# Kernel optimization log

Hardware: AMD Instinct MI355X
Metric: run time of the kernel (lower is better)

The kernel has to match this reference:

```python
import jax, jax.numpy as jnp
import numpy as np

D_MODEL, D_STATE, EXPAND = 1024, 16, 2
D_INNER = D_MODEL * EXPAND
BATCH, SEQ = 4, 2048
DT = 0.1

def setup_inputs() -> dict:
    key = jax.random.key(0)
    ks = jax.random.split(key, 12)
    s = 0.02
    inp = {
        "x": jax.random.normal(ks[0], (BATCH, SEQ, D_MODEL), jnp.float32),
        "B_mod": jax.random.normal(ks[1], (BATCH, D_STATE), jnp.float32) * 0.1,
        "C_mod": jax.random.normal(ks[2], (BATCH, D_STATE), jnp.float32) * 0.1,
        "W_in": jax.random.normal(ks[3], (D_MODEL, 2 * D_INNER), jnp.float32) * s,
        "b_in": jnp.zeros((2 * D_INNER,), jnp.float32),
        "conv_w": jax.random.normal(ks[4], (D_INNER, 1, 3), jnp.float32) * 0.3,
        "conv_b": jnp.zeros((D_INNER,), jnp.float32),
        "A_log": jnp.tile(jnp.log(jnp.arange(1, D_STATE + 1, dtype=jnp.float32))[None, :], (D_INNER, 1)),
        "D": jnp.ones((D_INNER,), jnp.float32),
        "W_B": jax.random.normal(ks[5], (D_INNER, D_STATE), jnp.float32) * s,
        "b_B": jnp.zeros((D_STATE,), jnp.float32),
        "W_C": jax.random.normal(ks[6], (D_INNER, D_STATE), jnp.float32) * s,
        "b_C": jnp.zeros((D_STATE,), jnp.float32),
        "W_out": jax.random.normal(ks[7], (D_INNER, D_MODEL), jnp.float32) * s,
        "b_out": jnp.zeros((D_MODEL,), jnp.float32),
    }
    return inp

def _silu(v):
    return v * jax.nn.sigmoid(v)

def reference(x, B_mod, C_mod, W_in, b_in, conv_w, conv_b, A_log, D, W_B, b_B, W_C, b_C, W_out, b_out):
    # in_proj + split + gate
    xr = x @ W_in + b_in                      # (B, L, 2*D_INNER)
    x_ssm, x_res = jnp.split(xr, 2, axis=-1)
    x_ssm = _silu(x_ssm)
    # depthwise conv1d, kernel 3, padding 1
    xc = jnp.transpose(x_ssm, (0, 2, 1))      # (B, C, L)
    xc = jax.lax.conv_general_dilated(
        xc, conv_w, window_strides=(1,), padding=[(1, 1)],
        dimension_numbers=("NCH", "OIH", "NCH"), feature_group_count=D_INNER)
    xc = xc + conv_b[None, :, None]
    x_ssm = jnp.transpose(xc, (0, 2, 1))      # (B, L, D_INNER)
    # SSM params
    A = -jnp.exp(A_log)                       # (D_INNER, D_STATE)
    A_bar = jnp.exp(A * DT)
    B = x_ssm @ W_B + b_B + B_mod[:, None, :] # (B, L, D_STATE)
    C = x_ssm @ W_C + b_C + C_mod[:, None, :]
    # sequential scan over time
    def step(h, inp):
        xt, Bt, Ct = inp                      # (B,D_INNER), (B,S), (B,S)
        h = A_bar[None] * h + xt[:, :, None] * Bt[:, None, :]
        yt = jnp.einsum("bds,bs->bd", h, Ct)
        return h, yt
    h0 = jnp.zeros((x.shape[0], D_INNER, D_STATE), x.dtype)
    xs = (jnp.moveaxis(x_ssm, 1, 0), jnp.moveaxis(B, 1, 0), jnp.moveaxis(C, 1, 0))
    _, ys = jax.lax.scan(step, h0, xs)        # (L, B, D_INNER)
    y = jnp.moveaxis(ys, 0, 1) + D[None, None, :] * x_ssm
    y = y * _silu(x_res)
    return y @ W_out + b_out
```

## Files before the change

kernel.cpp:

```cpp
#include <hip/hip_runtime.h>
#include <stdint.h>

#define D_MODEL 1024
#define D_STATE 16
#define D_INNER 2048
#define BATCH   4
#define SEQ     2048
#define ML      (BATCH*SEQ)
#define CH      64
#define NCHUNK  (SEQ/CH)
#define KSEG    8

typedef unsigned short u16;
typedef u16   u16x8  __attribute__((ext_vector_type(8)));
typedef short s16x8  __attribute__((ext_vector_type(8)));
typedef float f32x4  __attribute__((ext_vector_type(4)));

__device__ __forceinline__ float b2f(u16 u){
  union { uint32_t i; float f; } v; v.i = ((uint32_t)u) << 16; return v.f;
}
__device__ __forceinline__ u16 f2b(float f){
  uint32_t x = __float_as_uint(f);
  return (u16)((x + 0x7fffu + ((x >> 16) & 1u)) >> 16);
}
__device__ __forceinline__ float silu_f(float v){
  return v / (1.f + __expf(-v));
}
__device__ __forceinline__ void gl_lds16(const void* gp, void* lp){
  __builtin_amdgcn_global_load_lds(
      (const __attribute__((address_space(1))) void*)gp,
      (__attribute__((address_space(3))) void*)lp, 16, 0, 0);
}

__global__ __launch_bounds__(256) void transpose_cast_k(const float* __restrict__ in,
                                                        u16* __restrict__ out,
                                                        int R, int C){
  __shared__ float tile[32][33];
  int bx = blockIdx.x * 32, by = blockIdx.y * 32;
  int tx = threadIdx.x & 31, ty = threadIdx.x >> 5;
  #pragma unroll
  for (int i = 0; i < 32; i += 8)
    tile[ty + i][tx] = in[(size_t)(by + ty + i) * C + bx + tx];
  __syncthreads();
  #pragma unroll
  for (int i = 0; i < 32; i += 8)
    out[(size_t)(bx + ty + i) * R + by + tx] = f2b(tile[tx][ty + i]);
}

__global__ __launch_bounds__(256) void cast_k(const float* __restrict__ in,
                                              u16* __restrict__ out){
  size_t i = ((size_t)blockIdx.x * 256 + threadIdx.x) * 8;
  f32x4 a = *(const f32x4*)(in + i);
  f32x4 b = *(const f32x4*)(in + i + 4);
  u16x8 o;
  #pragma unroll
  for (int j = 0; j < 4; ++j){ o[j] = f2b(a[j]); o[4+j] = f2b(b[j]); }
  *(u16x8*)(out + i) = o;
}

__global__ __launch_bounds__(256) void bc_wt_k(const float* __restrict__ W_B,
                                               const float* __restrict__ W_C,
                                               u16* __restrict__ Wt){
  int n = blockIdx.y;
  int k = blockIdx.x * 256 + threadIdx.x;
  const float* src = (n < 16) ? W_B : W_C;
  Wt[(size_t)n * D_INNER + k] = f2b(src[(size_t)k * 16 + (n & 15)]);
}

#define G1_K  1024
#define G1_NT (G1_K/64)

__global__ __launch_bounds__(512, 2) void gemm1_k(const u16* __restrict__ A,
                                                  const u16* __restrict__ Bt,
                                                  const float* __restrict__ bias,
                                                  u16* __restrict__ out0,
                                                  u16* __restrict__ out1){
  __shared__ __align__(16) u16 ldsAll[256*264];
  u16* ldsA = ldsAll;
  u16* ldsB = ldsAll + 4*8192;

  const int bid = blockIdx.x;
  const int xcd = bid & 7, t2 = bid >> 3;
  const int n0 = (xcd*2 + (t2 & 1)) * 256;
  const int m0 = (t2 >> 1) * 256;

  const int tid  = threadIdx.x;
  const int wave = tid >> 6, lane = tid & 63;
  const int wr = wave >> 2;
  const int wc = wave & 3;
  const int lrow = lane & 15;
  const int q    = lane >> 4;

  const int cx0  = ((q ^ (lrow & 7)) << 3);
  const int cx1  = cx0 ^ 32;
  const int arow = lrow * 64;

  const int srow = lane >> 3;
  const int scol = (((lane & 7) ^ (lane >> 3)) << 3);

  auto stageA = [&](int buf, int h, int k0){
    const u16* s = A + (size_t)(m0 + h*128 + wave*16 + srow) * G1_K + k0 + scol;
    u16* d = ldsA + (buf*2 + h)*8192 + wave*1024;
    gl_lds16(s,                  d);
    gl_lds16(s + (size_t)8*G1_K, d + 512);
  };
  auto stageB = [&](int buf, int h, int k0){
    const u16* s = Bt + (size_t)(n0 + h*128 + wave*16 + srow) * G1_K + k0 + scol;
    u16* d = ldsB + (buf*2 + h)*8192 + wave*1024;
    gl_lds16(s,                  d);
    gl_lds16(s + (size_t)8*G1_K, d + 512);
  };

  f32x4 acc[8][4];
  #pragma unroll
  for (int i = 0; i < 8; ++i)
    #pragma unroll
    for (int j = 0; j < 4; ++j) acc[i][j] = (f32x4){0.f,0.f,0.f,0.f};

  s16x8 aA[2][2], aB[2][2];
  s16x8 bX[4][2], bY[4][2];

  #define READ_AQ(dst, Q, nb)                                            \
    { const u16* p_ = ldsA + ((nb)*2 + wr)*8192 + (Q)*2048 + arow;       \
      dst[0][0] = *(const s16x8*)(p_ + cx0);                             \
      dst[0][1] = *(const s16x8*)(p_ + cx1);                             \
      dst[1][0] = *(const s16x8*)(p_ + 1024 + cx0);                      \
      dst[1][1] = *(const s16x8*)(p_ + 1024 + cx1); }
  #define READ_B8(dst, nb)                                               \
    { const u16* p_ = ldsB + ((nb)*2 + (wc>>1))*8192 + (wc&1)*4096 + arow; \
      _Pragma("unroll")                                                  \
      for (int nj_ = 0; nj_ < 4; ++nj_){                                 \
        dst[nj_][0] = *(const s16x8*)(p_ + nj_*1024 + cx0);              \
        dst[nj_][1] = *(const s16x8*)(p_ + nj_*1024 + cx1); } }
  #define MFMA_Q(Q, AF, BF)                                              \
    { _Pragma("unroll")                                                  \
      for (int nj_ = 0; nj_ < 4; ++nj_){                                 \
        _Pragma("unroll")                                                \
        for (int kk_ = 0; kk_ < 2; ++kk_){                               \
          acc[2*(Q)][nj_]   = __builtin_amdgcn_mfma_f32_16x16x32_bf16(AF[0][kk_], BF[nj_][kk_], acc[2*(Q)][nj_],   0,0,0); \
          acc[2*(Q)+1][nj_] = __builtin_amdgcn_mfma_f32_16x16x32_bf16(AF[1][kk_], BF[nj_][kk_], acc[2*(Q)+1][nj_], 0,0,0); } } }

  stageA(0,0,0); stageA(0,1,0); stageB(0,0,0); stageB(0,1,0);
  stageB(1,0,64); stageB(1,1,64);
  asm volatile("s_waitcnt vmcnt(4)" ::: "memory");
  __builtin_amdgcn_s_barrier();
  __builtin_amdgcn_sched_barrier(0);
  READ_B8(bX, 0);
  READ_AQ(aA, 0, 0);

  auto tile_body = [&](int tt, int buf, s16x8 (&bC)[4][2], s16x8 (&bN)[4][2]){
    const int k1 = (tt+1 < G1_NT ? tt+1 : G1_NT-1) * 64;
    const int k2 = (tt+2 < G1_NT ? tt+2 : G1_NT-1) * 64;
    const int nb = buf ^ 1;

    READ_AQ(aB, 1, buf);
    stageA(nb, 1, k1);
    stageA(nb, 0, k1);
    __builtin_amdgcn_s_barrier();
    asm volatile("s_waitcnt lgkmcnt(4)" ::: "memory");
    __builtin_amdgcn_sched_barrier(0);
    __builtin_amdgcn_s_setprio(1);
    MFMA_Q(0, aA, bC);
    __builtin_amdgcn_s_setprio(0);
    __builtin_amdgcn_s_barrier();

    READ_AQ(aA, 2, buf);
    stageB(buf, 0, k2);
    __builtin_amdgcn_s_barrier();
    asm volatile("s_waitcnt lgkmcnt(4)" ::: "memory");
    __builtin_amdgcn_sched_barrier(0);
    __builtin_amdgcn_s_setprio(1);
    MFMA_Q(1, aB, bC);
    __builtin_amdgcn_s_setprio(0);
    __builtin_amdgcn_s_barrier();

    READ_AQ(aB, 3, buf);
    stageB(buf, 1, k2);
    __builtin_amdgcn_s_barrier();
    asm volatile("s_waitcnt lgkmcnt(4)" ::: "memory");
    __builtin_amdgcn_sched_barrier(0);
    __builtin_amdgcn_s_setprio(1);
    MFMA_Q(2, aA, bC);
    __builtin_amdgcn_s_setprio(0);
    __builtin_amdgcn_s_barrier();

    asm volatile("s_waitcnt vmcnt(4)" ::: "memory");
    __builtin_amdgcn_s_barrier();
    __builtin_amdgcn_sched_barrier(0);
    READ_B8(bN, nb);
    READ_AQ(aA, 0, nb);
    asm volatile("s_waitcnt lgkmcnt(12)" ::: "memory");
    __builtin_amdgcn_sched_barrier(0);
    __builtin_amdgcn_s_setprio(1);
    MFMA_Q(3, aB, bC);
    __builtin_amdgcn_s_setprio(0);
    __builtin_amdgcn_s_barrier();
  };

  for (int tt2 = 0; tt2 < G1_NT; tt2 += 2) {
    tile_body(tt2,     0, bX, bY);
    tile_body(tt2 + 1, 1, bY, bX);
  }

  asm volatile("s_waitcnt vmcnt(0)" ::: "memory");
  __syncthreads();

  #pragma unroll
  for (int nj = 0; nj < 4; ++nj) {
    const int colg = n0 + wc*64 + nj*16 + lrow;
    const float bv = bias[colg];
    const int coll = wc*64 + nj*16 + lrow;
    #pragma unroll
    for (int mi = 0; mi < 8; ++mi) {
      #pragma unroll
      for (int r = 0; r < 4; ++r) {
        const int rowl = wr*128 + mi*16 + q*4 + r;
        ldsAll[rowl*264 + coll] = f2b(silu_f(acc[mi][nj][r] + bv));
      }
    }
  }
  __syncthreads();

  u16* op = (n0 < D_INNER) ? out0 : out1;
  const int colbase = n0 & (D_INNER - 1);
  #pragma unroll
  for (int it = 0; it < 16; ++it) {
    const int f   = it*512 + tid;
    const int row = f >> 5;
    const int ch  = f & 31;
    u16x8 v = *(const u16x8*)(ldsAll + row*264 + ch*8);
    *(u16x8*)(op + (size_t)(m0 + row)*D_INNER + colbase + ch*8) = v;
  }
  #undef READ_AQ
  #undef READ_B8
  #undef MFMA_Q
}

template<int MODE>
__global__ __launch_bounds__(256) void gemm_bt(const u16* __restrict__ A,
                                               const u16* __restrict__ Bt,
                                               const float* __restrict__ bias,
                                               u16* __restrict__ out0,
                                               u16* __restrict__ out1,
                                               float* __restrict__ outf,
                                               int M, int N, int K, int n_per_xcd){
  __shared__ __align__(16) u16 Asb[2][128*32];
  __shared__ __align__(16) u16 Bsb[2][128*32];
  const int bid = blockIdx.x;
  const int xcd = bid & 7, t2 = bid >> 3;
  const int n0 = (xcd * n_per_xcd + (t2 % n_per_xcd)) * 128;
  const int m0 = (t2 / n_per_xcd) * 128;
  const int t    = threadIdx.x;
  const int wave = t >> 6, lane = t & 63;
  const int wm   = (wave >> 1) * 64, wn = (wave & 1) * 64;
  const int lrow = lane & 15, kq = (lane >> 4) * 8;
  const int srow = lane >> 2;
  const int scol = (lane & 3) * 8;

  f32x4 acc[4][4];
  #pragma unroll
  for (int i = 0; i < 4; ++i)
    #pragma unroll
    for (int j = 0; j < 4; ++j)
      acc[i][j] = (f32x4){0.f, 0.f, 0.f, 0.f};

  auto stage = [&](int buf, int k0){
    #pragma unroll
    for (int i = 0; i < 2; ++i) {
      int R0 = (wave*2 + i) * 16;
      gl_lds16(&A [(size_t)(m0 + R0 + srow)*K + k0 + scol], &Asb[buf][R0*32]);
      gl_lds16(&Bt[(size_t)(n0 + R0 + srow)*K + k0 + scol], &Bsb[buf][R0*32]);
    }
  };

  const int KT = K >> 5;
  stage(0, 0);
  __syncthreads();
  for (int kt = 0; kt < KT; ++kt) {
    const int cur = kt & 1;
    if (kt + 1 < KT) stage(1 - cur, (kt + 1) * 32);
    s16x8 af[4], bfr[4];
    #pragma unroll
    for (int i = 0; i < 4; ++i) af[i]  = *(const s16x8*)&Asb[cur][(wm + i*16 + lrow)*32 + kq];
    #pragma unroll
    for (int j = 0; j < 4; ++j) bfr[j] = *(const s16x8*)&Bsb[cur][(wn + j*16 + lrow)*32 + kq];
    #pragma unroll
    for (int i = 0; i < 4; ++i)
      #pragma unroll
      for (int j = 0; j < 4; ++j)
        acc[i][j] = __builtin_amdgcn_mfma_f32_16x16x32_bf16(af[i], bfr[j], acc[i][j], 0, 0, 0);
    __syncthreads();
  }

  const int Nh = N >> 1;
  #pragma unroll
  for (int i = 0; i < 4; ++i) {
    #pragma unroll
    for (int j = 0; j < 4; ++j) {
      int col = n0 + wn + j*16 + lrow;
      float bv = bias[col];
      #pragma unroll
      for (int r = 0; r < 4; ++r) {
        int row = m0 + wm + i*16 + (lane >> 4)*4 + r;
        float v = acc[i][j][r] + bv;
        if (MODE == 0) {
          outf[(size_t)row * N + col] = v;
        } else {
          float s = silu_f(v);
          if (col < Nh) out0[(size_t)row * Nh + col]        = f2b(s);
          else          out1[(size_t)row * Nh + (col - Nh)] = f2b(s);
        }
      }
    }
  }
}

__global__ __launch_bounds__(256) void bc_gemm_k(const u16* __restrict__ xs,
                                                 const float* __restrict__ conv_w,
                                                 const float* __restrict__ conv_b,
                                                 const u16* __restrict__ Wt,
                                                 float* __restrict__ partial){
  __shared__ __align__(16) u16 Rsb[130*40];
  __shared__ __align__(16) u16 Asb[128*40];
  __shared__ __align__(16) u16 Wsb[32*40];
  const int kseg = blockIdx.x;
  const int m0   = blockIdx.y * 128;
  const int t    = threadIdx.x;
  const int wave = t >> 6, lane = t & 63;
  const int wm   = wave * 32;
  const int lrow = lane & 15, kq = (lane >> 4) * 8;
  const bool zfirst = (m0 & (SEQ-1)) == 0;
  const bool zlast  = ((m0+128) & (SEQ-1)) == 0;
  const int ccol = t & 31, r0c = (t >> 5) * 16;

  f32x4 acc[2][2];
  #pragma unroll
  for (int i = 0; i < 2; ++i)
    #pragma unroll
    for (int j = 0; j < 2; ++j)
      acc[i][j] = (f32x4){0.f, 0.f, 0.f, 0.f};

  const int kbase = kseg * (D_INNER / KSEG);
  for (int ks = 0; ks < (D_INNER / KSEG); ks += 32) {
    int k0 = kbase + ks;
    if (t < 128) {
      int f = t * 8;
      int r = f >> 5, c = f & 31;
      *(u16x8*)&Wsb[r*40 + c] = *(const u16x8*)&Wt[(size_t)r*D_INNER + k0 + c];
    }
    #pragma unroll
    for (int i = 0; i < 3; ++i) {
      int idx = i*256 + t;
      if (idx < 520) {
        int r = idx >> 2, c = (idx & 3) * 8;
        u16x8 v = (u16x8){0,0,0,0,0,0,0,0};
        bool zero = (r == 0 && zfirst) || (r == 129 && zlast);
        if (!zero)
          v = *(const u16x8*)&xs[(size_t)(m0 - 1 + r)*D_INNER + k0 + c];
        *(u16x8*)&Rsb[r*40 + c] = v;
      }
    }
    __syncthreads();
    {
      const int dcol = k0 + ccol;
      const float cw0 = conv_w[dcol*3], cw1 = conv_w[dcol*3+1], cw2 = conv_w[dcol*3+2];
      const float cbv = conv_b[dcol];
      #pragma unroll
      for (int r = 0; r < 16; ++r) {
        int rr = r0c + r;
        float v = cw0 * b2f(Rsb[rr*40 + ccol])
                + cw1 * b2f(Rsb[(rr+1)*40 + ccol])
                + cw2 * b2f(Rsb[(rr+2)*40 + ccol]) + cbv;
        Asb[rr*40 + ccol] = f2b(v);
      }
    }
    __syncthreads();
    s16x8 af[2], wf[2];
    #pragma unroll
    for (int i = 0; i < 2; ++i) af[i] = *(const s16x8*)&Asb[(wm + i*16 + lrow)*40 + kq];
    #pragma unroll
    for (int j = 0; j < 2; ++j) wf[j] = *(const s16x8*)&Wsb[(j*16 + lrow)*40 + kq];
    #pragma unroll
    for (int i = 0; i < 2; ++i)
      #pragma unroll
      for (int j = 0; j < 2; ++j)
        acc[i][j] = __builtin_amdgcn_mfma_f32_16x16x32_bf16(af[i], wf[j], acc[i][j], 0, 0, 0);
    __syncthreads();
  }

  #pragma unroll
  for (int i = 0; i < 2; ++i)
    #pragma unroll
    for (int j = 0; j < 2; ++j)
      #pragma unroll
      for (int r = 0; r < 4; ++r) {
        int row = m0 + wm + i*16 + (lane >> 4)*4 + r;
        int col = j*16 + lrow;
        partial[((size_t)kseg * ML + row) * 32 + col] = acc[i][j][r];
      }
}

__global__ __launch_bounds__(256) void bc_reduce_k(const float* __restrict__ partial,
    const float* __restrict__ b_B, const float* __restrict__ B_mod,
    const float* __restrict__ b_C, const float* __restrict__ C_mod,
    float* __restrict__ Bbuf, float* __restrict__ Cbuf){
  int g = blockIdx.x * 256 + threadIdx.x;
  int row = g >> 5, col = g & 31;
  int b = row >> 11;
  float s = 0.f;
  #pragma unroll
  for (int seg = 0; seg < KSEG; ++seg)
    s += partial[(size_t)seg * ML * 32 + g];
  if (col < 16) Bbuf[(size_t)row*16 + col]      = s + b_B[col]      + B_mod[b*16 + col];
  else          Cbuf[(size_t)row*16 + col - 16] = s + b_C[col - 16] + C_mod[b*16 + col - 16];
}

__global__ __launch_bounds__(256) void state_k(const u16* __restrict__ xs,
    const float* __restrict__ conv_w, const float* __restrict__ conv_b,
    const float* __restrict__ Bbuf, const float* __restrict__ A_log,
    float* __restrict__ hend){
  int c = blockIdx.x, db = blockIdx.y, b = blockIdx.z;
  int d = db*256 + threadIdx.x;

  float Abar[16];
  #pragma unroll
  for (int s = 0; s < 16; ++s)
    Abar[s] = __expf(-0.1f * __expf(A_log[d*16 + s]));
  float h[16];
  #pragma unroll
  for (int s = 0; s < 16; ++s) h[s] = 0.f;

  const float w0 = conv_w[d*3], w1 = conv_w[d*3+1], w2 = conv_w[d*3+2], cb = conv_b[d];
  size_t base = (size_t)b * SEQ * D_INNER + (size_t)c * CH * D_INNER + d;
  const float* Br = Bbuf + ((size_t)b * SEQ + (size_t)c * CH) * 16;
  const int l0 = c * CH;

  float xm = (l0 > 0) ? b2f(xs[base - D_INNER]) : 0.f;
  float x0 = b2f(xs[base]);
  float xp = b2f(xs[base + D_INNER]);
  float Bc[16];
  #pragma unroll
  for (int s = 0; s < 16; ++s) Bc[s] = Br[s];

  for (int l = 0; l < CH; ++l){
    float xq = 0.f;
    if (l0 + l + 2 < SEQ) xq = b2f(xs[base + (size_t)(l+2)*D_INNER]);
    float Bl[16];
    #pragma unroll
    for (int s = 0; s < 16; ++s) Bl[s] = Bc[s];
    if (l < CH-1){
      #pragma unroll
      for (int s = 0; s < 16; ++s) Bc[s] = Br[(l+1)*16 + s];
    }
    float xc = w0*xm + w1*x0 + w2*xp + cb;
    #pragma unroll
    for (int s = 0; s < 16; ++s)
      h[s] = Abar[s]*h[s] + xc*Bl[s];
    xm = x0; x0 = xp; xp = xq;
  }
  float* hp = hend + (((size_t)(b*NCHUNK + c))*D_INNER + d)*16;
  #pragma unroll
  for (int q = 0; q < 4; ++q)
    *(f32x4*)(hp + q*4) = (f32x4){h[q*4], h[q*4+1], h[q*4+2], h[q*4+3]};
}

__global__ __launch_bounds__(256) void prefix_k(const float* __restrict__ hend,
    const float* __restrict__ A_log, float* __restrict__ hin){
  int g = blockIdx.x*256 + threadIdx.x;
  int s = g & 15;
  int d = (g >> 4) & (D_INNER-1);
  int b = g >> 15;
  float decay = __expf(-0.1f * (float)CH * __expf(A_log[d*16 + s]));
  size_t stride = (size_t)D_INNER * 16;
  const float* he = hend + (size_t)b*NCHUNK*stride + (size_t)d*16 + s;
  float*       hi = hin  + (size_t)b*NCHUNK*stride + (size_t)d*16 + s;
  float h = 0.f;
  for (int c0 = 0; c0 < NCHUNK; c0 += 8){
    float v[8];
    #pragma unroll
    for (int i = 0; i < 8; ++i) v[i] = he[(size_t)(c0+i)*stride];
    #pragma unroll
    for (int i = 0; i < 8; ++i){
      hi[(size_t)(c0+i)*stride] = h;
      h = decay*h + v[i];
    }
  }
}

__global__ __launch_bounds__(256) void scan2_k(const u16* __restrict__ xs,
    const u16* __restrict__ gate,
    const float* __restrict__ conv_w, const float* __restrict__ conv_b,
    const float* __restrict__ Bbuf, const float* __restrict__ Cbuf,
    const float* __restrict__ A_log, const float* __restrict__ Dp,
    const float* __restrict__ hin, u16* __restrict__ ybuf){
  int c = blockIdx.x, db = blockIdx.y, b = blockIdx.z;
  int d = db*256 + threadIdx.x;

  float Abar[16];
  #pragma unroll
  for (int s = 0; s < 16; ++s)
    Abar[s] = __expf(-0.1f * __expf(A_log[d*16 + s]));
  float h[16];
  const float* hp = hin + (((size_t)(b*NCHUNK + c))*D_INNER + d)*16;
  #pragma unroll
  for (int q = 0; q < 4; ++q){
    f32x4 v = *(const f32x4*)(hp + q*4);
    #pragma unroll
    for (int j = 0; j < 4; ++j) h[q*4 + j] = v[j];
  }
  float Dd = Dp[d];
  const float w0 = conv_w[d*3], w1 = conv_w[d*3+1], w2 = conv_w[d*3+2], cb = conv_b[d];

  size_t base = (size_t)b * SEQ * D_INNER + (size_t)c * CH * D_INNER + d;
  const float* Br = Bbuf + ((size_t)b * SEQ + (size_t)c * CH) * 16;
  const float* Cr = Cbuf + ((size_t)b * SEQ + (size_t)c * CH) * 16;
  const int l0 = c * CH;

  float xm = (l0 > 0) ? b2f(xs[base - D_INNER]) : 0.f;
  float x0 = b2f(xs[base]);
  float xp = b2f(xs[base + D_INNER]);
  float Bc[16], Cc[16];
  #pragma unroll
  for (int s = 0; s < 16; ++s){ Bc[s] = Br[s]; Cc[s] = Cr[s]; }
  float gcur = b2f(gate[base]);

  for (int l = 0; l < CH; ++l){
    float xq = 0.f;
    if (l0 + l + 2 < SEQ) xq = b2f(xs[base + (size_t)(l+2)*D_INNER]);
    float gnext = (l < CH-1) ? b2f(gate[base + (size_t)(l+1)*D_INNER]) : 0.f;
    float Bl[16], Cl[16];
    #pragma unroll
    for (int s = 0; s < 16; ++s){ Bl[s] = Bc[s]; Cl[s] = Cc[s]; }
    if (l < CH-1){
      #pragma unroll
      for (int s = 0; s < 16; ++s){ Bc[s] = Br[(l+1)*16 + s]; Cc[s] = Cr[(l+1)*16 + s]; }
    }
    float xc = w0*xm + w1*x0 + w2*xp + cb;
    float ya[4] = {0.f, 0.f, 0.f, 0.f};
    #pragma unroll
    for (int s = 0; s < 16; ++s){
      float hv = Abar[s]*h[s] + xc*Bl[s];
      h[s] = hv;
      ya[s & 3] += hv * Cl[s];
    }
    float y = ((ya[0]+ya[1]) + (ya[2]+ya[3]) + Dd*xc) * gcur;
    ybuf[base + (size_t)l*D_INNER] = f2b(y);
    xm = x0; x0 = xp; xp = xq; gcur = gnext;
  }
}

extern "C" void kernel_launch(void* const* d_in, const int* in_sizes, int n_in,
                              void* d_out, int out_size, void* d_ws, size_t ws_size,
                              hipStream_t stream){
  const float* x      = (const float*)d_in[0];
  const float* B_mod  = (const float*)d_in[1];
  const float* C_mod  = (const float*)d_in[2];
  const float* W_in   = (const float*)d_in[3];
  const float* b_in   = (const float*)d_in[4];
  const float* conv_w = (const float*)d_in[5];
  const float* conv_b = (const float*)d_in[6];
  const float* A_log  = (const float*)d_in[7];
  const float* Dp     = (const float*)d_in[8];
  const float* W_B    = (const float*)d_in[9];
  const float* b_B    = (const float*)d_in[10];
  const float* W_C    = (const float*)d_in[11];
  const float* b_C    = (const float*)d_in[12];
  const float* W_out  = (const float*)d_in[13];
  const float* b_out  = (const float*)d_in[14];
  float* out = (float*)d_out;

  char* ws = (char*)d_ws;
  size_t off = 0;
  auto alloc = [&](size_t bytes)->char* {
    char* p = ws + off; off += (bytes + 255) & ~(size_t)255; return p;
  };
  u16* Wt_in  = (u16*)alloc((size_t)(2*D_INNER)*D_MODEL*2);
  u16* Wt_out = (u16*)alloc((size_t)D_MODEL*D_INNER*2);
  u16* xs     = (u16*)alloc((size_t)ML*D_INNER*2);
  u16* gatep  = (u16*)alloc((size_t)ML*D_INNER*2);
  u16* ybuf   = (u16*)alloc((size_t)ML*D_INNER*2);
  float* Bbuf = (float*)alloc((size_t)ML*D_STATE*4);
  float* Cbuf = (float*)alloc((size_t)ML*D_STATE*4);
  u16* xbf    = (u16*)alloc((size_t)ML*D_MODEL*2);
  float* hin  = (float*)alloc((size_t)BATCH*NCHUNK*D_INNER*16*4);
  u16* Wt_bc  = (u16*)alloc((size_t)32*D_INNER*2);
  float* hend    = (float*)xbf;
  float* partial = (float*)Wt_in;

  transpose_cast_k<<<dim3((2*D_INNER)/32, D_MODEL/32), 256, 0, stream>>>(W_in, Wt_in, D_MODEL, 2*D_INNER);
  transpose_cast_k<<<dim3(D_MODEL/32, D_INNER/32),     256, 0, stream>>>(W_out, Wt_out, D_INNER, D_MODEL);
  cast_k<<<dim3((ML*D_MODEL)/(256*8)), 256, 0, stream>>>(x, xbf);
  bc_wt_k<<<dim3(D_INNER/256, 32), 256, 0, stream>>>(W_B, W_C, Wt_bc);

  gemm1_k<<<dim3(512), 512, 0, stream>>>(xbf, Wt_in, b_in, xs, gatep);

  bc_gemm_k<<<dim3(KSEG, ML/128), 256, 0, stream>>>(xs, conv_w, conv_b, Wt_bc, partial);
  bc_reduce_k<<<dim3((ML*32)/256), 256, 0, stream>>>(
      partial, b_B, B_mod, b_C, C_mod, Bbuf, Cbuf);

  state_k<<<dim3(NCHUNK, D_INNER/256, BATCH), 256, 0, stream>>>(
      xs, conv_w, conv_b, Bbuf, A_log, hend);
  prefix_k<<<dim3((BATCH*D_INNER*16)/256), 256, 0, stream>>>(hend, A_log, hin);
  scan2_k<<<dim3(NCHUNK, D_INNER/256, BATCH), 256, 0, stream>>>(
      xs, gatep, conv_w, conv_b, Bbuf, Cbuf, A_log, Dp, hin, ybuf);

  gemm_bt<0><<<dim3(512), 256, 0, stream>>>(
      ybuf, Wt_out, b_out, nullptr, nullptr, out, ML, D_MODEL, D_INNER, 1);
}
```

Before: 368.8 us.

## Merge prep kernels, double scan chunk size, restage gemm1 A-tile prefetch

Merges the four weight and input cast/transpose kernels into a single prep launch with block-index dispatch, which removes launch gaps. Doubles the scan chunk length, halving the number of chunks and the size of the cross-chunk prefix work while lengthening each chunk's sequential loop. Reorders the gemm1 pipeline so the A tile is prefetched two tiles ahead, like B, with an added barrier before the A staging. The A-buffer reuse timing changes, which adds a risk of race conditions.

```diff
diff --git a/kernel.cpp b/kernel.cpp
--- a/kernel.cpp
+++ b/kernel.cpp
@@ -7,7 +7,7 @@
 #define BATCH   4
 #define SEQ     2048
 #define ML      (BATCH*SEQ)
-#define CH      64
+#define CH      128
 #define NCHUNK  (SEQ/CH)
 #define KSEG    8
 
@@ -32,39 +32,47 @@
       (__attribute__((address_space(3))) void*)lp, 16, 0, 0);
 }
 
-__global__ __launch_bounds__(256) void transpose_cast_k(const float* __restrict__ in,
-                                                        u16* __restrict__ out,
-                                                        int R, int C){
+__global__ __launch_bounds__(256) void prep_k(const float* __restrict__ W_in,
+                                              const float* __restrict__ W_out,
+                                              const float* __restrict__ x,
+                                              const float* __restrict__ W_B,
+                                              const float* __restrict__ W_C,
+                                              u16* __restrict__ Wt_in,
+                                              u16* __restrict__ Wt_out,
+                                              u16* __restrict__ xbf,
+                                              u16* __restrict__ Wt_bc){
   __shared__ float tile[32][33];
-  int bx = blockIdx.x * 32, by = blockIdx.y * 32;
-  int tx = threadIdx.x & 31, ty = threadIdx.x >> 5;
-  #pragma unroll
-  for (int i = 0; i < 32; i += 8)
-    tile[ty + i][tx] = in[(size_t)(by + ty + i) * C + bx + tx];
-  __syncthreads();
-  #pragma unroll
-  for (int i = 0; i < 32; i += 8)
-    out[(size_t)(bx + ty + i) * R + by + tx] = f2b(tile[tx][ty + i]);
-}
-
-__global__ __launch_bounds__(256) void cast_k(const float* __restrict__ in,
-                                              u16* __restrict__ out){
-  size_t i = ((size_t)blockIdx.x * 256 + threadIdx.x) * 8;
-  f32x4 a = *(const f32x4*)(in + i);
-  f32x4 b = *(const f32x4*)(in + i + 4);
-  u16x8 o;
-  #pragma unroll
-  for (int j = 0; j < 4; ++j){ o[j] = f2b(a[j]); o[4+j] = f2b(b[j]); }
-  *(u16x8*)(out + i) = o;
-}
-
-__global__ __launch_bounds__(256) void bc_wt_k(const float* __restrict__ W_B,
-                                               const float* __restrict__ W_C,
-                                               u16* __restrict__ Wt){
-  int n = blockIdx.y;
-  int k = blockIdx.x * 256 + threadIdx.x;
-  const float* src = (n < 16) ? W_B : W_C;
-  Wt[(size_t)n * D_INNER + k] = f2b(src[(size_t)k * 16 + (n & 15)]);
+  int bb = blockIdx.x;
+  if (bb < 6144) {
+    const float* in; u16* out; int R, C, bx, by;
+    if (bb < 4096) { in = W_in;  out = Wt_in;  R = 1024; C = 4096;
+                     bx = (bb & 127) * 32; by = (bb >> 7) * 32; }
+    else { bb -= 4096; in = W_out; out = Wt_out; R = 2048; C = 1024;
+                     bx = (bb & 31) * 32; by = (bb >> 5) * 32; }
+    int tx = threadIdx.x & 31, ty = threadIdx.x >> 5;
+    #pragma unroll
+    for (int i = 0; i < 32; i += 8)
+      tile[ty + i][tx] = in[(size_t)(by + ty + i) * C + bx + tx];
+    __syncthreads();
+    #pragma unroll
+    for (int i = 0; i < 32; i += 8)
+      out[(size_t)(bx + ty + i) * R + by + tx] = f2b(tile[tx][ty + i]);
+  } else if (bb < 10240) {
+    bb -= 6144;
+    size_t i = ((size_t)bb * 256 + threadIdx.x) * 8;
+    f32x4 a = *(const f32x4*)(x + i);
+    f32x4 b = *(const f32x4*)(x + i + 4);
+    u16x8 o;
+    #pragma unroll
+    for (int j = 0; j < 4; ++j){ o[j] = f2b(a[j]); o[4+j] = f2b(b[j]); }
+    *(u16x8*)(xbf + i) = o;
+  } else {
+    bb -= 10240;
+    int n = bb >> 3;
+    int k = (bb & 7) * 256 + threadIdx.x;
+    const float* src = (n < 16) ? W_B : W_C;
+    Wt_bc[(size_t)n * D_INNER + k] = f2b(src[(size_t)k * 16 + (n & 15)]);
+  }
 }
 
 #define G1_K  1024
@@ -140,22 +148,19 @@
           acc[2*(Q)][nj_]   = __builtin_amdgcn_mfma_f32_16x16x32_bf16(AF[0][kk_], BF[nj_][kk_], acc[2*(Q)][nj_],   0,0,0); \
           acc[2*(Q)+1][nj_] = __builtin_amdgcn_mfma_f32_16x16x32_bf16(AF[1][kk_], BF[nj_][kk_], acc[2*(Q)+1][nj_], 0,0,0); } } }
 
-  stageA(0,0,0); stageA(0,1,0); stageB(0,0,0); stageB(0,1,0);
-  stageB(1,0,64); stageB(1,1,64);
-  asm volatile("s_waitcnt vmcnt(4)" ::: "memory");
+  stageB(0,0,0); stageB(0,1,0); stageA(0,0,0); stageA(0,1,0);
+  stageB(1,0,64); stageB(1,1,64); stageA(1,0,64); stageA(1,1,64);
+  asm volatile("s_waitcnt vmcnt(8)" ::: "memory");
   __builtin_amdgcn_s_barrier();
   __builtin_amdgcn_sched_barrier(0);
   READ_B8(bX, 0);
   READ_AQ(aA, 0, 0);
 
   auto tile_body = [&](int tt, int buf, s16x8 (&bC)[4][2], s16x8 (&bN)[4][2]){
-    const int k1 = (tt+1 < G1_NT ? tt+1 : G1_NT-1) * 64;
     const int k2 = (tt+2 < G1_NT ? tt+2 : G1_NT-1) * 64;
     const int nb = buf ^ 1;
 
     READ_AQ(aB, 1, buf);
-    stageA(nb, 1, k1);
-    stageA(nb, 0, k1);
     __builtin_amdgcn_s_barrier();
     asm volatile("s_waitcnt lgkmcnt(4)" ::: "memory");
     __builtin_amdgcn_sched_barrier(0);
@@ -191,6 +196,9 @@
     READ_AQ(aA, 0, nb);
     asm volatile("s_waitcnt lgkmcnt(12)" ::: "memory");
     __builtin_amdgcn_sched_barrier(0);
+    __builtin_amdgcn_s_barrier();
+    stageA(buf, 0, k2);
+    stageA(buf, 1, k2);
     __builtin_amdgcn_s_setprio(1);
     MFMA_Q(3, aB, bC);
     __builtin_amdgcn_s_setprio(0);
@@ -587,10 +595,8 @@
   float* hend    = (float*)xbf;
   float* partial = (float*)Wt_in;
 
-  transpose_cast_k<<<dim3((2*D_INNER)/32, D_MODEL/32), 256, 0, stream>>>(W_in, Wt_in, D_MODEL, 2*D_INNER);
-  transpose_cast_k<<<dim3(D_MODEL/32, D_INNER/32),     256, 0, stream>>>(W_out, Wt_out, D_INNER, D_MODEL);
-  cast_k<<<dim3((ML*D_MODEL)/(256*8)), 256, 0, stream>>>(x, xbf);
-  bc_wt_k<<<dim3(D_INNER/256, 32), 256, 0, stream>>>(W_B, W_C, Wt_bc);
+  prep_k<<<dim3(10496), 256, 0, stream>>>(W_in, W_out, x, W_B, W_C,
+                                          Wt_in, Wt_out, xbf, Wt_bc);
 
   gemm1_k<<<dim3(512), 512, 0, stream>>>(xbf, Wt_in, b_in, xs, gatep);
 
```

After: 425.7 us. +15.4%, slower.
